# Optimization experiments

Hardware: AMD Instinct MI355X
Metric: run time of the kernel (lower is better)

The kernel has to match this reference:

```python
import jax, jax.numpy as jnp
import numpy as np

KERNEL = 25
PAD = (KERNEL - 1) // 2  # 12
LN_EPS = 1e-5
CAP_FACTOR = 2.0
K_VALUE = 2


def _moving_avg(x):
    # x: [B, L, D]; Autoformer moving_avg: replicate-pad ends, avg-pool k=25 stride 1
    front = jnp.repeat(x[:, :1, :], PAD, axis=1)
    end = jnp.repeat(x[:, -1:, :], PAD, axis=1)
    xp = jnp.concatenate([front, x, end], axis=1)            # [B, L+2*PAD, D]
    cs = jnp.cumsum(xp, axis=1)
    cs = jnp.concatenate([jnp.zeros_like(cs[:, :1]), cs], axis=1)
    return (cs[:, KERNEL:] - cs[:, :-KERNEL]) / KERNEL        # [B, L, D]


def _layernorm(h, g, b):
    mu = jnp.mean(h, axis=-1, keepdims=True)
    d = h - mu
    var = jnp.mean(d * d, axis=-1, keepdims=True)
    return d * jax.lax.rsqrt(var + LN_EPS) * g + b


def setup_inputs() -> dict:
    key = jax.random.key(0)
    ks = jax.random.split(key, 6)
    B, L, D, H, E = 32, 512, 512, 1024, 8
    sd_in = 1.0 / np.sqrt(D)
    sd_h = 1.0 / np.sqrt(H)
    return {
        "x": jax.random.normal(ks[0], (B, L, D), jnp.float32),
        "Wt": jax.random.normal(ks[1], (D, H), jnp.float32) * sd_in,
        "bt": jax.random.normal(ks[2], (H,), jnp.float32) * sd_in,
        "gt": jnp.ones((H,), jnp.float32),
        "bet": jnp.zeros((H,), jnp.float32),
        "Ws": jax.random.normal(ks[3], (D, H), jnp.float32) * sd_in,
        "bs": jax.random.normal(ks[4], (H,), jnp.float32) * sd_in,
        "gs": jnp.ones((H,), jnp.float32),
        "bes": jnp.zeros((H,), jnp.float32),
        "W2": jax.random.normal(ks[5], (H, E), jnp.float32) * sd_h,
        "b2": jnp.zeros((E,), jnp.float32),
    }


def reference(x, Wt, bt, gt, bet, Ws, bs, gs, bes, W2, b2):
    # series decomposition: (residual, moving_mean) -> (trend_init, seasonal_init)
    ma = _moving_avg(x)
    trend_init = x - ma          # residual (first return of series_decomp)
    seasonal_init = ma           # moving mean (second return)

    t = _layernorm(trend_init @ Wt + bt, gt, bet)       # [B, L, H]
    s = _layernorm(seasonal_init @ Ws + bs, gs, bes)    # [B, L, H]
    med = jax.nn.relu(t + s)
    logits = med @ W2 + b2                               # [B, L, E]
    gate_scores = jax.nn.softmax(logits, axis=-1)

    B, L, E = gate_scores.shape
    capacity = int(CAP_FACTOR * B)

    _, top_k_indices = jax.lax.top_k(gate_scores, K_VALUE)  # [B, L, K]
    # torch scatter_(1, idx, 1) on 3D: mask[b, idx[b,l,j], j] = 1
    bi = jnp.arange(B)[:, None, None]
    ji = jnp.arange(K_VALUE)[None, None, :]
    mask = jnp.zeros_like(gate_scores).at[bi, top_k_indices, ji].set(1.0)

    masked = gate_scores * mask
    denom = jnp.sum(masked, axis=0, keepdims=True) + 1e-4    # [1, L, E]
    return masked / denom * capacity
```

## Files before the change

kernel.cpp:

```cpp
#include <hip/hip_runtime.h>

#define NB 32
#define NL 512
#define ND 512
#define NH 1024
#define NE 8
#define NROWS (NB * NL)
#define CW 2048
#define SPAD 136

typedef __attribute__((ext_vector_type(8))) short bf16x8;
typedef __attribute__((ext_vector_type(4))) float f32x4;
typedef __attribute__((ext_vector_type(4))) unsigned u32x4;

__device__ __forceinline__ unsigned short f2bf(float f) {
    unsigned u = __float_as_uint(f);
    return (unsigned short)((u + 0x7fffu + ((u >> 16) & 1u)) >> 16);
}
__device__ __forceinline__ float bf2f(unsigned short b) {
    return __uint_as_float(((unsigned)b) << 16);
}
__device__ __forceinline__ unsigned pktr(float a, float b) {
    return (__float_as_uint(a) >> 16) | (__float_as_uint(b) & 0xFFFF0000u);
}

__global__ __launch_bounds__(256) void wprep(
    const float* __restrict__ Wt, const float* __restrict__ Ws,
    unsigned* __restrict__ bpack)
{
    __shared__ float tile[64][65];
    int bid = blockIdx.x;
    int mat = bid >> 7, rem = bid & 127;
    int kt0 = (rem >> 4) << 6;
    int nt0 = (rem & 15) << 6;
    const float* W = mat ? Ws : Wt;
    unsigned* Oh = bpack;
    unsigned* Ol = bpack + 524288u;
    int t = threadIdx.x;
    #pragma unroll
    for (int i = 0; i < 16; ++i) {
        int idx = t + 256 * i;
        int k = idx >> 6, n = idx & 63;
        tile[k][n] = W[(size_t)(kt0 + k) * NH + nt0 + n];
    }
    __syncthreads();
    #pragma unroll
    for (int i = 0; i < 8; ++i) {
        int idx = t + 256 * i;
        int jp = idx & 3, lane = (idx >> 2) & 63, kbr = (idx >> 8) & 1, ntr = (idx >> 9) & 3;
        int ncol = ntr * 16 + (lane & 15);
        int kcol = kbr * 32 + ((lane >> 4) << 3) + jp * 2;
        float w0 = tile[kcol][ncol], w1 = tile[kcol + 1][ncol];
        unsigned short h0 = f2bf(w0), h1 = f2bf(w1);
        unsigned short l0 = f2bf(w0 - bf2f(h0)), l1 = f2bf(w1 - bf2f(h1));
        int ntg = mat * 64 + (nt0 >> 4) + ntr;
        int kb = (kt0 >> 5) + kbr;
        unsigned offs = ((unsigned)(ntg * 16 + kb) * 64u + (unsigned)lane) * 4u + jp;
        Oh[offs] = (unsigned)h0 | ((unsigned)h1 << 16);
        Ol[offs] = (unsigned)l0 | ((unsigned)l1 << 16);
    }
}

__global__ __launch_bounds__(512, 4) void gemm_all(
    const float* __restrict__ x, const unsigned* __restrict__ bpack,
    unsigned short* __restrict__ C, unsigned short* __restrict__ Clo)
{
    __shared__ union {
        unsigned short A[2][128][64];
        unsigned short cs[64][264];
    } sm;

    const int tid = threadIdx.x, lane = tid & 63, wave = tid >> 6;
    const int g = lane >> 4, c = lane & 15;

    if (blockIdx.x < 1024) {
        const int wm = wave >> 2, wn = wave & 3;
        const int bid = blockIdx.x;
        const int xcd = bid & 7, idx = bid >> 3;
        const int mi = xcd * 16 + (idx >> 3), ni = idx & 7;
        const int m0 = mi * 128;

        const int srow = tid >> 2, sj = tid & 3;
        const int wcol = (sj * 8) ^ ((srow & 7) << 3);
        const float* xs = x + (size_t)(m0 + srow) * ND + sj * 8;

        f32x4 acc[4][4];
        #pragma unroll
        for (int nf = 0; nf < 4; ++nf)
            #pragma unroll
            for (int mf = 0; mf < 4; ++mf) acc[nf][mf] = (f32x4){0.f, 0.f, 0.f, 0.f};

        float4 xa = *(const float4*)xs;
        float4 xb = *(const float4*)(xs + 4);

        int p = 0;
        for (int kb = 0; kb < 16; ++kb) {
            u32x4 u;
            u.x = pktr(xa.x, xa.y); u.y = pktr(xa.z, xa.w);
            u.z = pktr(xb.x, xb.y); u.w = pktr(xb.z, xb.w);
            *(u32x4*)&sm.A[p][srow][wcol] = u;
            if (kb < 15) {
                const float* pn = xs + (kb + 1) * 32;
                xa = *(const float4*)pn;
                xb = *(const float4*)(pn + 4);
            }
            __syncthreads();

            bf16x8 af[4];
            #pragma unroll
            for (int mf = 0; mf < 4; ++mf) {
                int R = wm * 64 + mf * 16 + c;
                int rcol = (g * 8) ^ ((R & 7) << 3);
                af[mf] = *(const bf16x8*)&sm.A[p][R][rcol];
            }
            #pragma unroll
            for (int nf = 0; nf < 4; ++nf) {
                int nt = ni * 16 + wn * 4 + nf;
                bf16x8 bfr = *(const bf16x8*)(bpack + ((size_t)(nt * 16 + kb) * 64 + lane) * 4);
                #pragma unroll
                for (int mf = 0; mf < 4; ++mf)
                    acc[nf][mf] = __builtin_amdgcn_mfma_f32_16x16x32_bf16(af[mf], bfr, acc[nf][mf], 0, 0, 0);
            }
            p ^= 1;
        }

        #pragma unroll
        for (int ph = 0; ph < 2; ++ph) {
            __syncthreads();
            if (wm == ph) {
                #pragma unroll
                for (int nf = 0; nf < 4; ++nf)
                    #pragma unroll
                    for (int mf = 0; mf < 4; ++mf)
                        #pragma unroll
                        for (int r = 0; r < 4; ++r)
                            sm.cs[mf * 16 + g * 4 + r][wn * 64 + nf * 16 + c] =
                                (unsigned short)(__float_as_uint(acc[nf][mf][r]) >> 16);
            }
            __syncthreads();
            int row = tid >> 3, ch = tid & 7;
            int grow = m0 + ph * 64 + row;
            if ((grow & 511) >= 32) {
                unsigned short* dst = &C[(size_t)grow * CW + ni * 256 + ch * 32];
                #pragma unroll
                for (int q = 0; q < 4; ++q)
                    *(uint4*)(dst + q * 8) = *(const uint4*)&sm.cs[row][ch * 32 + q * 8];
            }
        }
    } else {
        const int eb = blockIdx.x - 1024;
        const int bq = eb >> 3, ni = eb & 7;
        const int m0 = bq * NL;
        const unsigned* Bhi = bpack;
        const unsigned* Blo = bpack + 524288u;

        f32x4 acc[4][2];
        #pragma unroll
        for (int nf = 0; nf < 4; ++nf)
            #pragma unroll
            for (int mf = 0; mf < 2; ++mf) acc[nf][mf] = (f32x4){0.f, 0.f, 0.f, 0.f};

        if (tid < 256) {
            const float* xr0 = x + (size_t)(m0 + c) * ND + g * 8;
            #pragma unroll 2
            for (int kb = 0; kb < 16; ++kb) {
                bf16x8 ah[2], al[2];
                #pragma unroll
                for (int mf = 0; mf < 2; ++mf) {
                    const float* p = xr0 + mf * (16 * ND) + kb * 32;
                    float4 a0 = *(const float4*)p;
                    float4 a1 = *(const float4*)(p + 4);
                    float f[8] = {a0.x, a0.y, a0.z, a0.w, a1.x, a1.y, a1.z, a1.w};
                    float lo[8];
                    #pragma unroll
                    for (int j = 0; j < 8; ++j) {
                        float hif = __uint_as_float(__float_as_uint(f[j]) & 0xFFFF0000u);
                        lo[j] = f[j] - hif;
                    }
                    u32x4 uh, ul;
                    uh.x = pktr(f[0], f[1]); uh.y = pktr(f[2], f[3]);
                    uh.z = pktr(f[4], f[5]); uh.w = pktr(f[6], f[7]);
                    ul.x = pktr(lo[0], lo[1]); ul.y = pktr(lo[2], lo[3]);
                    ul.z = pktr(lo[4], lo[5]); ul.w = pktr(lo[6], lo[7]);
                    ah[mf] = __builtin_bit_cast(bf16x8, uh);
                    al[mf] = __builtin_bit_cast(bf16x8, ul);
                }
                #pragma unroll
                for (int nf = 0; nf < 4; ++nf) {
                    int nt = ni * 16 + wave * 4 + nf;
                    size_t bo = ((size_t)(nt * 16 + kb) * 64 + lane) * 4;
                    bf16x8 bh = *(const bf16x8*)(Bhi + bo);
                    bf16x8 bl = *(const bf16x8*)(Blo + bo);
                    #pragma unroll
                    for (int mf = 0; mf < 2; ++mf) {
                        acc[nf][mf] = __builtin_amdgcn_mfma_f32_16x16x32_bf16(ah[mf], bh, acc[nf][mf], 0, 0, 0);
                        acc[nf][mf] = __builtin_amdgcn_mfma_f32_16x16x32_bf16(al[mf], bh, acc[nf][mf], 0, 0, 0);
                        acc[nf][mf] = __builtin_amdgcn_mfma_f32_16x16x32_bf16(ah[mf], bl, acc[nf][mf], 0, 0, 0);
                    }
                }
            }
            #pragma unroll
            for (int nf = 0; nf < 4; ++nf)
                #pragma unroll
                for (int mf = 0; mf < 2; ++mf)
                    #pragma unroll
                    for (int r = 0; r < 4; ++r)
                        sm.cs[mf * 16 + g * 4 + r][wave * 64 + nf * 16 + c] =
                            (unsigned short)(__float_as_uint(acc[nf][mf][r]) >> 16);
        }
        __syncthreads();
        if (tid < 256) {
            #pragma unroll
            for (int i = 0; i < 4; ++i) {
                int idx = tid + 256 * i;
                int row = idx >> 5, cg = idx & 31;
                *(uint4*)&C[(size_t)(m0 + row) * CW + ni * 256 + cg * 8] = *(const uint4*)&sm.cs[row][cg * 8];
            }
        }
        __syncthreads();
        if (tid < 256) {
            #pragma unroll
            for (int nf = 0; nf < 4; ++nf)
                #pragma unroll
                for (int mf = 0; mf < 2; ++mf)
                    #pragma unroll
                    for (int r = 0; r < 4; ++r) {
                        float v = acc[nf][mf][r];
                        float hif = __uint_as_float(__float_as_uint(v) & 0xFFFF0000u);
                        sm.cs[mf * 16 + g * 4 + r][wave * 64 + nf * 16 + c] =
                            (unsigned short)(__float_as_uint(v - hif) >> 16);
                    }
        }
        __syncthreads();
        if (tid < 256) {
            #pragma unroll
            for (int i = 0; i < 3; ++i) {
                int idx = tid + 256 * i;
                int row = idx >> 5, cg = idx & 31;
                if (row < 20)
                    *(uint4*)&Clo[((size_t)bq * 20 + row) * CW + ni * 256 + cg * 8] = *(const uint4*)&sm.cs[row][cg * 8];
            }
        }
    }
}

__global__ __launch_bounds__(256) void stats_all(
    const unsigned short* __restrict__ C, const unsigned short* __restrict__ Clo,
    const float* __restrict__ bt, const float* __restrict__ bs,
    float* __restrict__ rowpart, float* __restrict__ exstat)
{
    __shared__ unsigned short stg[88][SPAD];
    const int tid = threadIdx.x;

    if (blockIdx.x < 1024) {
        const int bid = blockIdx.x;
        const int q = bid & 3, lc = (bid >> 2) & 7, b = bid >> 5;
        const int l0 = lc * 64;
        const int cq = tid & 31, rg = tid >> 5;
        const float inv25 = 1.f / 25.f;

        float s[8], qa[8];
        #pragma unroll
        for (int r = 0; r < 8; ++r) { s[r] = 0.f; qa[r] = 0.f; }

        for (int ch = 0; ch < 4; ++ch) {
            int cb = q * 512 + ch * 128;
            __syncthreads();
            for (int i = tid; i < 1408; i += 256) {
                int si = i >> 4, cg = i & 15;
                int gl = l0 - 12 + si;
                gl = gl < 0 ? 0 : (gl > NL - 1 ? NL - 1 : gl);
                *(uint4*)&stg[si][cg * 8] = *(const uint4*)&C[(size_t)(b * NL + gl) * CW + cb + cg * 8];
            }
            __syncthreads();

            float bv[4];
            {
                float4 b4 = q < 2 ? *(const float4*)&bt[cb + cq * 4]
                                  : *(const float4*)&bs[cb - 1024 + cq * 4];
                bv[0] = b4.x; bv[1] = b4.y; bv[2] = b4.z; bv[3] = b4.w;
            }
            float run[4] = {0.f, 0.f, 0.f, 0.f};
            #pragma unroll
            for (int w = 0; w < 25; ++w) {
                ushort4 u = *(const ushort4*)&stg[rg * 8 + w][cq * 4];
                run[0] += bf2f(u.x); run[1] += bf2f(u.y); run[2] += bf2f(u.z); run[3] += bf2f(u.w);
            }
            #pragma unroll
            for (int rr = 0; rr < 8; ++rr) {
                if (rr > 0) {
                    ushort4 un = *(const ushort4*)&stg[rg * 8 + rr + 24][cq * 4];
                    ushort4 uo = *(const ushort4*)&stg[rg * 8 + rr - 1][cq * 4];
                    run[0] += bf2f(un.x) - bf2f(uo.x); run[1] += bf2f(un.y) - bf2f(uo.y);
                    run[2] += bf2f(un.z) - bf2f(uo.z); run[3] += bf2f(un.w) - bf2f(uo.w);
                }
                float pre[4];
                if (q < 2) {
                    ushort4 uc = *(const ushort4*)&stg[rg * 8 + rr + 12][cq * 4];
                    pre[0] = bf2f(uc.x) - run[0] * inv25 + bv[0];
                    pre[1] = bf2f(uc.y) - run[1] * inv25 + bv[1];
                    pre[2] = bf2f(uc.z) - run[2] * inv25 + bv[2];
                    pre[3] = bf2f(uc.w) - run[3] * inv25 + bv[3];
                } else {
                    pre[0] = run[0] * inv25 + bv[0];
                    pre[1] = run[1] * inv25 + bv[1];
                    pre[2] = run[2] * inv25 + bv[2];
                    pre[3] = run[3] * inv25 + bv[3];
                }
                s[rr]  += pre[0] + pre[1] + pre[2] + pre[3];
                qa[rr] += pre[0] * pre[0] + pre[1] * pre[1] + pre[2] * pre[2] + pre[3] * pre[3];
            }
        }

        #pragma unroll
        for (int rr = 0; rr < 8; ++rr)
            #pragma unroll
            for (int o = 1; o < 32; o <<= 1) {
                s[rr]  += __shfl_xor(s[rr], o);
                qa[rr] += __shfl_xor(qa[rr], o);
            }
        if (cq == 0) {
            #pragma unroll
            for (int rr = 0; rr < 8; ++rr) {
                size_t gr = (size_t)b * NL + l0 + rg * 8 + rr;
                rowpart[(gr * 4 + q) * 2 + 0] = s[rr];
                rowpart[(gr * 4 + q) * 2 + 1] = qa[rr];
            }
        }
    } else {
        const int inst = (blockIdx.x - 1024) * 4 + (tid >> 6);
        const int b = inst >> 3, chunk = inst & 7;
        const int t = tid & 63;
        const int c4 = chunk * 256 + t * 4;
        const bool isU = chunk < 4;
        const float inv25 = 1.f / 25.f;

        float bias[4];
        {
            float4 b4 = isU ? *(const float4*)&bt[c4] : *(const float4*)&bs[c4 - 1024];
            bias[0] = b4.x; bias[1] = b4.y; bias[2] = b4.z; bias[3] = b4.w;
        }
        float s[8], q[8];
        #pragma unroll
        for (int r = 0; r < 8; ++r) { s[r] = 0.f; q[r] = 0.f; }

        float cs[4] = {0, 0, 0, 0}, v0[4], keep[8][4];
        #pragma unroll
        for (int j = 0; j < 20; ++j) {
            ushort4 h  = *(const ushort4*)&C[(size_t)(b * NL + j) * CW + c4];
            ushort4 lo = *(const ushort4*)&Clo[((size_t)b * 20 + j) * CW + c4];
            float u[4] = {bf2f(h.x) + bf2f(lo.x), bf2f(h.y) + bf2f(lo.y),
                          bf2f(h.z) + bf2f(lo.z), bf2f(h.w) + bf2f(lo.w)};
            if (j == 0) {
                #pragma unroll
                for (int k = 0; k < 4; ++k) v0[k] = u[k];
            }
            if (j < 8) {
                #pragma unroll
                for (int k = 0; k < 4; ++k) keep[j][k] = u[k];
            }
            #pragma unroll
            for (int k = 0; k < 4; ++k) cs[k] += u[k];
            if (j >= 12) {
                const int l = j - 12;
                const float w0 = (float)(24 - j);
                #pragma unroll
                for (int k = 0; k < 4; ++k) {
                    float ma = (cs[k] + w0 * v0[k]) * inv25;
                    float pre = isU ? (keep[l][k] - ma + bias[k]) : (ma + bias[k]);
                    s[l] += pre;
                    q[l] += pre * pre;
                }
            }
        }
        #pragma unroll
        for (int r = 0; r < 8; ++r)
            #pragma unroll
            for (int o = 1; o < 64; o <<= 1) {
                s[r] += __shfl_xor(s[r], o);
                q[r] += __shfl_xor(q[r], o);
            }
        if (t == 0) {
            #pragma unroll
            for (int r = 0; r < 8; ++r) {
                exstat[(((size_t)b * 8 + chunk) * 8 + r) * 2 + 0] = s[r];
                exstat[(((size_t)b * 8 + chunk) * 8 + r) * 2 + 1] = q[r];
            }
        }
    }
}

__global__ __launch_bounds__(64) void exact_apply(
    const unsigned short* __restrict__ C, const unsigned short* __restrict__ Clo,
    const float* __restrict__ bt, const float* __restrict__ gt, const float* __restrict__ bet,
    const float* __restrict__ bs, const float* __restrict__ gs, const float* __restrict__ bes,
    const float* __restrict__ W2, const float* __restrict__ exstat,
    float* __restrict__ exlg)
{
    const int t = threadIdx.x;
    const int chunk = blockIdx.x & 7, b = blockIdx.x >> 3;
    const int h2 = chunk * 128 + t * 2;
    const float inv25 = 1.f / 25.f;

    float mu_t[8], rs_t[8], mu_s[8], rs_s[8];
    #pragma unroll
    for (int l = 0; l < 8; ++l) {
        float st = 0.f, qt = 0.f, ss = 0.f, qs = 0.f;
        #pragma unroll
        for (int ch = 0; ch < 4; ++ch) {
            st += exstat[(((size_t)b * 8 + ch) * 8 + l) * 2 + 0];
            qt += exstat[(((size_t)b * 8 + ch) * 8 + l) * 2 + 1];
            ss += exstat[(((size_t)b * 8 + 4 + ch) * 8 + l) * 2 + 0];
            qs += exstat[(((size_t)b * 8 + 4 + ch) * 8 + l) * 2 + 1];
        }
        mu_t[l] = st * (1.f / NH);
        rs_t[l] = rsqrtf(qt * (1.f / NH) - mu_t[l] * mu_t[l] + 1e-5f);
        mu_s[l] = ss * (1.f / NH);
        rs_s[l] = rsqrtf(qs * (1.f / NH) - mu_s[l] * mu_s[l] + 1e-5f);
    }

    float btv[2], gtv[2], bev[2], bsv[2], gsv[2], besv[2], w2r[2][NE];
    #pragma unroll
    for (int k = 0; k < 2; ++k) {
        int h = h2 + k;
        btv[k] = bt[h]; gtv[k] = gt[h]; bev[k] = bet[h];
        bsv[k] = bs[h]; gsv[k] = gs[h]; besv[k] = bes[h];
        const float4* wp = (const float4*)&W2[(size_t)h * NE];
        float4 a = wp[0], c2 = wp[1];
        w2r[k][0] = a.x;  w2r[k][1] = a.y;  w2r[k][2] = a.z;  w2r[k][3] = a.w;
        w2r[k][4] = c2.x; w2r[k][5] = c2.y; w2r[k][6] = c2.z; w2r[k][7] = c2.w;
    }

    float csU[2] = {0, 0}, csV[2] = {0, 0}, v0U[2], v0V[2], keepU[8][2];
    float lg[8][NE];
    #pragma unroll
    for (int l = 0; l < 8; ++l)
        #pragma unroll
        for (int e = 0; e < NE; ++e) lg[l][e] = 0.f;

    #pragma unroll
    for (int j = 0; j < 20; ++j) {
        size_t rb = (size_t)(b * NL + j) * CW;
        size_t lb = ((size_t)b * 20 + j) * CW;
        ushort2 hu  = *(const ushort2*)&C[rb + h2];
        ushort2 lu  = *(const ushort2*)&Clo[lb + h2];
        ushort2 hv  = *(const ushort2*)&C[rb + NH + h2];
        ushort2 lv  = *(const ushort2*)&Clo[lb + NH + h2];
        float u[2] = {bf2f(hu.x) + bf2f(lu.x), bf2f(hu.y) + bf2f(lu.y)};
        float v[2] = {bf2f(hv.x) + bf2f(lv.x), bf2f(hv.y) + bf2f(lv.y)};
        if (j == 0) {
            #pragma unroll
            for (int k = 0; k < 2; ++k) { v0U[k] = u[k]; v0V[k] = v[k]; }
        }
        if (j < 8) {
            #pragma unroll
            for (int k = 0; k < 2; ++k) keepU[j][k] = u[k];
        }
        #pragma unroll
        for (int k = 0; k < 2; ++k) { csU[k] += u[k]; csV[k] += v[k]; }
        if (j >= 12) {
            const int l = j - 12;
            const float w0 = (float)(24 - j);
            #pragma unroll
            for (int k = 0; k < 2; ++k) {
                float maU = (csU[k] + w0 * v0U[k]) * inv25;
                float maV = (csV[k] + w0 * v0V[k]) * inv25;
                float tn = ((keepU[l][k] - maU + btv[k]) - mu_t[l]) * rs_t[l] * gtv[k] + bev[k];
                float sn = ((maV + bsv[k]) - mu_s[l]) * rs_s[l] * gsv[k] + besv[k];
                float m = tn + sn; m = m > 0.f ? m : 0.f;
                #pragma unroll
                for (int e = 0; e < NE; ++e) lg[l][e] = fmaf(m, w2r[k][e], lg[l][e]);
            }
        }
    }
    #pragma unroll
    for (int l = 0; l < 8; ++l)
        #pragma unroll
        for (int e = 0; e < NE; ++e)
            #pragma unroll
            for (int o = 1; o < 64; o <<= 1)
                lg[l][e] += __shfl_xor(lg[l][e], o);
    if (t == 0) {
        #pragma unroll
        for (int l = 0; l < 8; ++l)
            #pragma unroll
            for (int e = 0; e < NE; ++e)
                exlg[(((size_t)b * 8 + chunk) * 8 + l) * NE + e] = lg[l][e];
    }
}

__global__ __launch_bounds__(256) void apply_k(
    const unsigned short* __restrict__ C,
    const float* __restrict__ bt, const float* __restrict__ gt, const float* __restrict__ bet,
    const float* __restrict__ bs, const float* __restrict__ gs, const float* __restrict__ bes,
    const float* __restrict__ W2, const float* __restrict__ rowpart,
    float* __restrict__ lgpart)
{
    __shared__ unsigned short stgU[88][SPAD];
    __shared__ unsigned short stgV[88][SPAD];
    __shared__ float4 rowstat[64];

    const int tid = threadIdx.x;
    const int bid = blockIdx.x;
    const int q = bid & 3, lc = (bid >> 2) & 7, b = bid >> 5;
    const int l0 = lc * 64;
    const int cq = tid & 31, rg = tid >> 5;
    const float inv25 = 1.f / 25.f;

    if (tid < 64) {
        size_t gr = (size_t)b * NL + l0 + tid;
        const float* p = &rowpart[gr * 8];
        float st = p[0] + p[2], qt = p[1] + p[3];
        float ss = p[4] + p[6], qs = p[5] + p[7];
        float mut = st * (1.f / NH), mus = ss * (1.f / NH);
        float vt = qt * (1.f / NH) - mut * mut;
        float vs = qs * (1.f / NH) - mus * mus;
        rowstat[tid] = make_float4(mut, rsqrtf(vt + 1e-5f), mus, rsqrtf(vs + 1e-5f));
    }

    float lgp[8][NE];
    #pragma unroll
    for (int r = 0; r < 8; ++r)
        #pragma unroll
        for (int e = 0; e < NE; ++e) lgp[r][e] = 0.f;

    for (int ch = 0; ch < 2; ++ch) {
        int hb = q * 256 + ch * 128;
        __syncthreads();
        for (int i = tid; i < 1408; i += 256) {
            int si = i >> 4, cg = i & 15;
            int gl = l0 - 12 + si;
            gl = gl < 0 ? 0 : (gl > NL - 1 ? NL - 1 : gl);
            size_t rb = (size_t)(b * NL + gl) * CW;
            *(uint4*)&stgU[si][cg * 8] = *(const uint4*)&C[rb + hb + cg * 8];
            *(uint4*)&stgV[si][cg * 8] = *(const uint4*)&C[rb + NH + hb + cg * 8];
        }
        __syncthreads();

        int col = hb + cq * 4;
        float4 btv = *(const float4*)&bt[col],  gtv = *(const float4*)&gt[col];
        float4 bev = *(const float4*)&bet[col], bsv = *(const float4*)&bs[col];
        float4 gsv = *(const float4*)&gs[col],  besv = *(const float4*)&bes[col];
        float btr[4] = {btv.x, btv.y, btv.z, btv.w};
        float gtr[4] = {gtv.x, gtv.y, gtv.z, gtv.w};
        float ber[4] = {bev.x, bev.y, bev.z, bev.w};
        float bsr[4] = {bsv.x, bsv.y, bsv.z, bsv.w};
        float gsr[4] = {gsv.x, gsv.y, gsv.z, gsv.w};
        float besr[4] = {besv.x, besv.y, besv.z, besv.w};
        float w2r[4][NE];
        #pragma unroll
        for (int j = 0; j < 4; ++j) {
            const float4* wp = (const float4*)&W2[(size_t)(col + j) * NE];
            float4 a = wp[0], c2 = wp[1];
            w2r[j][0] = a.x;  w2r[j][1] = a.y;  w2r[j][2] = a.z;  w2r[j][3] = a.w;
            w2r[j][4] = c2.x; w2r[j][5] = c2.y; w2r[j][6] = c2.z; w2r[j][7] = c2.w;
        }

        float runU[4] = {0.f, 0.f, 0.f, 0.f}, runV[4] = {0.f, 0.f, 0.f, 0.f};
        #pragma unroll
        for (int w = 0; w < 25; ++w) {
            ushort4 u = *(const ushort4*)&stgU[rg * 8 + w][cq * 4];
            ushort4 v = *(const ushort4*)&stgV[rg * 8 + w][cq * 4];
            runU[0] += bf2f(u.x); runU[1] += bf2f(u.y); runU[2] += bf2f(u.z); runU[3] += bf2f(u.w);
            runV[0] += bf2f(v.x); runV[1] += bf2f(v.y); runV[2] += bf2f(v.z); runV[3] += bf2f(v.w);
        }
        #pragma unroll
        for (int rr = 0; rr < 8; ++rr) {
            if (rr > 0) {
                ushort4 un = *(const ushort4*)&stgU[rg * 8 + rr + 24][cq * 4];
                ushort4 uo = *(const ushort4*)&stgU[rg * 8 + rr - 1][cq * 4];
                ushort4 vn = *(const ushort4*)&stgV[rg * 8 + rr + 24][cq * 4];
                ushort4 vo = *(const ushort4*)&stgV[rg * 8 + rr - 1][cq * 4];
                runU[0] += bf2f(un.x) - bf2f(uo.x); runU[1] += bf2f(un.y) - bf2f(uo.y);
                runU[2] += bf2f(un.z) - bf2f(uo.z); runU[3] += bf2f(un.w) - bf2f(uo.w);
                runV[0] += bf2f(vn.x) - bf2f(vo.x); runV[1] += bf2f(vn.y) - bf2f(vo.y);
                runV[2] += bf2f(vn.z) - bf2f(vo.z); runV[3] += bf2f(vn.w) - bf2f(vo.w);
            }
            float4 rs = rowstat[rg * 8 + rr];
            ushort4 uc = *(const ushort4*)&stgU[rg * 8 + rr + 12][cq * 4];
            float cen[4] = {bf2f(uc.x), bf2f(uc.y), bf2f(uc.z), bf2f(uc.w)};
            float med[4];
            #pragma unroll
            for (int j = 0; j < 4; ++j) {
                float tn = ((cen[j] - runU[j] * inv25 + btr[j]) - rs.x) * rs.y * gtr[j] + ber[j];
                float sn = ((runV[j] * inv25 + bsr[j]) - rs.z) * rs.w * gsr[j] + besr[j];
                float m = tn + sn;
                med[j] = m > 0.f ? m : 0.f;
            }
            #pragma unroll
            for (int e = 0; e < NE; ++e)
                lgp[rr][e] = fmaf(med[0], w2r[0][e], fmaf(med[1], w2r[1][e],
                             fmaf(med[2], w2r[2][e], fmaf(med[3], w2r[3][e], lgp[rr][e]))));
        }
    }

    #pragma unroll
    for (int rr = 0; rr < 8; ++rr)
        #pragma unroll
        for (int e = 0; e < NE; ++e)
            #pragma unroll
            for (int o = 1; o < 32; o <<= 1)
                lgp[rr][e] += __shfl_xor(lgp[rr][e], o);
    if (cq == 0) {
        #pragma unroll
        for (int rr = 0; rr < 8; ++rr) {
            size_t gr = (size_t)b * NL + l0 + rg * 8 + rr;
            #pragma unroll
            for (int e = 0; e < NE; ++e)
                lgpart[(gr * 4 + q) * NE + e] = lgp[rr][e];
        }
    }
}

__global__ __launch_bounds__(256) void final_all(
    const float* __restrict__ lgpart, const float* __restrict__ exlg,
    const float* __restrict__ b2,
    unsigned* __restrict__ mb, float* __restrict__ gates)
{
    const int t = threadIdx.x;
    if (blockIdx.x < 64) {
        int row = blockIdx.x * 256 + t;
        int b = row >> 9, l = row & (NL - 1);
        float lg[NE];
        #pragma unroll
        for (int e = 0; e < NE; ++e) lg[e] = b2[e];
        #pragma unroll
        for (int qq = 0; qq < 4; ++qq)
            #pragma unroll
            for (int e = 0; e < NE; ++e)
                lg[e] += lgpart[((size_t)row * 4 + qq) * NE + e];
        int i0 = 0;
        #pragma unroll
        for (int e = 1; e < NE; ++e) if (lg[e] > lg[i0]) i0 = e;
        int i1 = i0 == 0 ? 1 : 0;
        #pragma unroll
        for (int e = 0; e < NE; ++e) if (e != i0 && lg[e] > lg[i1]) i1 = e;
        unsigned m = (l < 8) ? 0u : ((1u << i0) | (1u << (8 + i1)));
        #pragma unroll
        for (int o = 1; o < 64; o <<= 1) m |= __shfl_xor(m, o);
        if ((t & 63) == 0) {
            atomicOr(&mb[2 * b + 0], m & 0xffu);
            atomicOr(&mb[2 * b + 1], m >> 8);
        }
    } else {
        const int b = t >> 3, l = t & 7;
        float lg[NE];
        #pragma unroll
        for (int e = 0; e < NE; ++e) lg[e] = b2[e];
        #pragma unroll
        for (int ch = 0; ch < 8; ++ch)
            #pragma unroll
            for (int e = 0; e < NE; ++e)
                lg[e] += exlg[(((size_t)b * 8 + ch) * 8 + l) * NE + e];
        float mx = lg[0];
        #pragma unroll
        for (int e = 1; e < NE; ++e) mx = lg[e] > mx ? lg[e] : mx;
        float p[NE]; float sum = 0.f;
        #pragma unroll
        for (int e = 0; e < NE; ++e) { p[e] = expf(lg[e] - mx); sum += p[e]; }
        float inv = 1.f / sum;
        #pragma unroll
        for (int e = 0; e < NE; ++e)
            gates[((size_t)b * 8 + l) * NE + e] = p[e] * inv;
        int i0 = 0;
        #pragma unroll
        for (int e = 1; e < NE; ++e) if (lg[e] > lg[i0]) i0 = e;
        int i1 = i0 == 0 ? 1 : 0;
        #pragma unroll
        for (int e = 0; e < NE; ++e) if (e != i0 && lg[e] > lg[i1]) i1 = e;
        unsigned m = (1u << i0) | (1u << (8 + i1));
        m |= __shfl_xor(m, 1); m |= __shfl_xor(m, 2); m |= __shfl_xor(m, 4);
        if (l == 0) {
            atomicOr(&mb[2 * b + 0], m & 0xffu);
            atomicOr(&mb[2 * b + 1], m >> 8);
        }
    }
}

__global__ void finalize_k(const unsigned* __restrict__ mb,
                           const float* __restrict__ gates,
                           float* __restrict__ out)
{
    int t = threadIdx.x;
    if (t >= 16) return;
    int l = t >> 1, e = t & 1;
    float m[NB];
    float sum = 0.f;
    #pragma unroll
    for (int bb = 0; bb < NB; ++bb) {
        float gvv = gates[((size_t)bb * 8 + l) * NE + e];
        float on  = ((mb[2 * bb + e] >> l) & 1u) ? 1.f : 0.f;
        m[bb] = gvv * on;
        sum += m[bb];
    }
    float scale = 64.f / (sum + 1e-4f);
    #pragma unroll
    for (int bb = 0; bb < NB; ++bb)
        out[(size_t)bb * (NL * NE) + l * NE + e] = m[bb] * scale;
}

extern "C" void kernel_launch(void* const* d_in, const int* in_sizes, int n_in,
                              void* d_out, int out_size, void* d_ws, size_t ws_size,
                              hipStream_t stream) {
    const float* x   = (const float*)d_in[0];
    const float* Wt  = (const float*)d_in[1];
    const float* bt  = (const float*)d_in[2];
    const float* gt  = (const float*)d_in[3];
    const float* bet = (const float*)d_in[4];
    const float* Ws  = (const float*)d_in[5];
    const float* bs  = (const float*)d_in[6];
    const float* gs  = (const float*)d_in[7];
    const float* bes = (const float*)d_in[8];
    const float* W2  = (const float*)d_in[9];
    const float* b2  = (const float*)d_in[10];
    float* out = (float*)d_out;

    char* wsb = (char*)d_ws;
    unsigned*       mbp     = (unsigned*)wsb;
    float*          gates   = (float*)(wsb + 256);
    unsigned*       bpack   = (unsigned*)(wsb + 4096);
    float*          rowpart = (float*)(wsb + 4096);
    float*          lgpart  = (float*)(wsb + 4096 + 524288);
    float*          exstat  = (float*)(wsb + 4096 + 524288 + 2097152);
    float*          exlg    = (float*)(wsb + 4096 + 524288 + 2097152 + 16384);
    unsigned short* C       = (unsigned short*)(wsb + 4096 + 4194304);
    unsigned short* Clo     = (unsigned short*)(wsb + 4096 + 4194304 + (size_t)NROWS * CW * 2);

    hipMemsetAsync(d_out, 0, sizeof(float) * NB * NL * NE, stream);
    hipMemsetAsync(mbp, 0, 256, stream);

    wprep<<<256, 256, 0, stream>>>(Wt, Ws, bpack);
    gemm_all<<<1280, 512, 0, stream>>>(x, bpack, C, Clo);
    stats_all<<<1088, 256, 0, stream>>>(C, Clo, bt, bs, rowpart, exstat);
    exact_apply<<<256, 64, 0, stream>>>(C, Clo, bt, gt, bet, bs, gs, bes, W2, exstat, exlg);
    apply_k<<<1024, 256, 0, stream>>>(C, bt, gt, bet, bs, gs, bes, W2, rowpart, lgpart);
    final_all<<<65, 256, 0, stream>>>(lgpart, exlg, b2, mbp, gates);
    finalize_k<<<1, 64, 0, stream>>>(mbp, gates, out);
}
```

Measured before the change: 176.5 us.

## Double GEMM block N-tile to 512 and use all waves in exact path

```diff
diff --git a/kernel.cpp b/kernel.cpp
--- a/kernel.cpp
+++ b/kernel.cpp
@@ -21,7 +21,7 @@
     return __uint_as_float(((unsigned)b) << 16);
 }
 __device__ __forceinline__ unsigned pktr(float a, float b) {
-    return (__float_as_uint(a) >> 16) | (__float_as_uint(b) & 0xFFFF0000u);
+    return __builtin_amdgcn_perm(__float_as_uint(b), __float_as_uint(a), 0x07060302u);
 }
 
 __global__ __launch_bounds__(256) void wprep(
@@ -73,22 +73,22 @@
     const int tid = threadIdx.x, lane = tid & 63, wave = tid >> 6;
     const int g = lane >> 4, c = lane & 15;
 
-    if (blockIdx.x < 1024) {
+    if (blockIdx.x < 512) {
         const int wm = wave >> 2, wn = wave & 3;
         const int bid = blockIdx.x;
         const int xcd = bid & 7, idx = bid >> 3;
-        const int mi = xcd * 16 + (idx >> 3), ni = idx & 7;
+        const int mi = xcd * 16 + (idx >> 2), ni = idx & 3;
         const int m0 = mi * 128;
+
+        f32x4 acc[8][4];
+        #pragma unroll
+        for (int nf = 0; nf < 8; ++nf)
+            #pragma unroll
+            for (int mf = 0; mf < 4; ++mf) acc[nf][mf] = (f32x4){0.f, 0.f, 0.f, 0.f};
 
         const int srow = tid >> 2, sj = tid & 3;
         const int wcol = (sj * 8) ^ ((srow & 7) << 3);
         const float* xs = x + (size_t)(m0 + srow) * ND + sj * 8;
-
-        f32x4 acc[4][4];
-        #pragma unroll
-        for (int nf = 0; nf < 4; ++nf)
-            #pragma unroll
-            for (int mf = 0; mf < 4; ++mf) acc[nf][mf] = (f32x4){0.f, 0.f, 0.f, 0.f};
 
         float4 xa = *(const float4*)xs;
         float4 xb = *(const float4*)(xs + 4);
@@ -114,8 +114,8 @@
                 af[mf] = *(const bf16x8*)&sm.A[p][R][rcol];
             }
             #pragma unroll
-            for (int nf = 0; nf < 4; ++nf) {
-                int nt = ni * 16 + wn * 4 + nf;
+            for (int nf = 0; nf < 8; ++nf) {
+                int nt = ni * 32 + wn * 8 + nf;
                 bf16x8 bfr = *(const bf16x8*)(bpack + ((size_t)(nt * 16 + kb) * 64 + lane) * 4);
                 #pragma unroll
                 for (int mf = 0; mf < 4; ++mf)
@@ -125,31 +125,33 @@
         }
 
         #pragma unroll
-        for (int ph = 0; ph < 2; ++ph) {
-            __syncthreads();
-            if (wm == ph) {
-                #pragma unroll
-                for (int nf = 0; nf < 4; ++nf)
+        for (int ph = 0; ph < 2; ++ph)
+            #pragma unroll
+            for (int chh = 0; chh < 2; ++chh) {
+                __syncthreads();
+                if (wm == ph && (wn >> 1) == chh) {
                     #pragma unroll
-                    for (int mf = 0; mf < 4; ++mf)
+                    for (int nf = 0; nf < 8; ++nf)
                         #pragma unroll
-                        for (int r = 0; r < 4; ++r)
-                            sm.cs[mf * 16 + g * 4 + r][wn * 64 + nf * 16 + c] =
-                                (unsigned short)(__float_as_uint(acc[nf][mf][r]) >> 16);
-            }
-            __syncthreads();
-            int row = tid >> 3, ch = tid & 7;
-            int grow = m0 + ph * 64 + row;
-            if ((grow & 511) >= 32) {
-                unsigned short* dst = &C[(size_t)grow * CW + ni * 256 + ch * 32];
-                #pragma unroll
-                for (int q = 0; q < 4; ++q)
-                    *(uint4*)(dst + q * 8) = *(const uint4*)&sm.cs[row][ch * 32 + q * 8];
-            }
-        }
+                        for (int mf = 0; mf < 4; ++mf)
+                            #pragma unroll
+                            for (int r = 0; r < 4; ++r)
+                                sm.cs[mf * 16 + g * 4 + r][(wn & 1) * 128 + nf * 16 + c] =
+                                    (unsigned short)(__float_as_uint(acc[nf][mf][r]) >> 16);
+                }
+                __syncthreads();
+                int row = tid >> 3, chv = tid & 7;
+                int grow = m0 + ph * 64 + row;
+                if ((grow & 511) >= 32) {
+                    unsigned short* dst = &C[(size_t)grow * CW + ni * 512 + chh * 256 + chv * 32];
+                    #pragma unroll
+                    for (int q = 0; q < 4; ++q)
+                        *(uint4*)(dst + q * 8) = *(const uint4*)&sm.cs[row][chv * 32 + q * 8];
+                }
+            }
     } else {
-        const int eb = blockIdx.x - 1024;
-        const int bq = eb >> 3, ni = eb & 7;
+        const int eb = blockIdx.x - 512;
+        const int bq = eb >> 2, nq = eb & 3;
         const int m0 = bq * NL;
         const unsigned* Bhi = bpack;
         const unsigned* Blo = bpack + 524288u;
@@ -160,85 +162,91 @@
             #pragma unroll
             for (int mf = 0; mf < 2; ++mf) acc[nf][mf] = (f32x4){0.f, 0.f, 0.f, 0.f};
 
-        if (tid < 256) {
-            const float* xr0 = x + (size_t)(m0 + c) * ND + g * 8;
-            #pragma unroll 2
-            for (int kb = 0; kb < 16; ++kb) {
-                bf16x8 ah[2], al[2];
+        const float* xr0 = x + (size_t)(m0 + c) * ND + g * 8;
+        #pragma unroll 2
+        for (int kb = 0; kb < 16; ++kb) {
+            bf16x8 ah[2], al[2];
+            #pragma unroll
+            for (int mf = 0; mf < 2; ++mf) {
+                const float* p = xr0 + mf * (16 * ND) + kb * 32;
+                float4 a0 = *(const float4*)p;
+                float4 a1 = *(const float4*)(p + 4);
+                float f[8] = {a0.x, a0.y, a0.z, a0.w, a1.x, a1.y, a1.z, a1.w};
+                float lo[8];
+                #pragma unroll
+                for (int j = 0; j < 8; ++j) {
+                    float hif = __uint_as_float(__float_as_uint(f[j]) & 0xFFFF0000u);
+                    lo[j] = f[j] - hif;
+                }
+                u32x4 uh, ul;
+                uh.x = pktr(f[0], f[1]); uh.y = pktr(f[2], f[3]);
+                uh.z = pktr(f[4], f[5]); uh.w = pktr(f[6], f[7]);
+                ul.x = pktr(lo[0], lo[1]); ul.y = pktr(lo[2], lo[3]);
+                ul.z = pktr(lo[4], lo[5]); ul.w = pktr(lo[6], lo[7]);
+                ah[mf] = __builtin_bit_cast(bf16x8, uh);
+                al[mf] = __builtin_bit_cast(bf16x8, ul);
+            }
+            #pragma unroll
+            for (int nf = 0; nf < 4; ++nf) {
+                int nt = nq * 32 + wave * 4 + nf;
+                size_t bo = ((size_t)(nt * 16 + kb) * 64 + lane) * 4;
+                bf16x8 bh = *(const bf16x8*)(Bhi + bo);
+                bf16x8 bl = *(const bf16x8*)(Blo + bo);
                 #pragma unroll
                 for (int mf = 0; mf < 2; ++mf) {
-                    const float* p = xr0 + mf * (16 * ND) + kb * 32;
-                    float4 a0 = *(const float4*)p;
-                    float4 a1 = *(const float4*)(p + 4);
-                    float f[8] = {a0.x, a0.y, a0.z, a0.w, a1.x, a1.y, a1.z, a1.w};
-                    float lo[8];
+                    acc[nf][mf] = __builtin_amdgcn_mfma_f32_16x16x32_bf16(ah[mf], bh, acc[nf][mf], 0, 0, 0);
+                    acc[nf][mf] = __builtin_amdgcn_mfma_f32_16x16x32_bf16(al[mf], bh, acc[nf][mf], 0, 0, 0);
+                    acc[nf][mf] = __builtin_amdgcn_mfma_f32_16x16x32_bf16(ah[mf], bl, acc[nf][mf], 0, 0, 0);
+                }
+            }
+        }
+
+        #pragma unroll
+        for (int ph = 0; ph < 2; ++ph) {
+            __syncthreads();
+            if ((wave >> 2) == ph) {
+                #pragma unroll
+                for (int nf = 0; nf < 4; ++nf)
                     #pragma unroll
-                    for (int j = 0; j < 8; ++j) {
-                        float hif = __uint_as_float(__float_as_uint(f[j]) & 0xFFFF0000u);
-                        lo[j] = f[j] - hif;
-                    }
-                    u32x4 uh, ul;
-                    uh.x = pktr(f[0], f[1]); uh.y = pktr(f[2], f[3]);
-                    uh.z = pktr(f[4], f[5]); uh.w = pktr(f[6], f[7]);
-                    ul.x = pktr(lo[0], lo[1]); ul.y = pktr(lo[2], lo[3]);
-                    ul.z = pktr(lo[4], lo[5]); ul.w = pktr(lo[6], lo[7]);
-                    ah[mf] = __builtin_bit_cast(bf16x8, uh);
-                    al[mf] = __builtin_bit_cast(bf16x8, ul);
-                }
-                #pragma unroll
-                for (int nf = 0; nf < 4; ++nf) {
-                    int nt = ni * 16 + wave * 4 + nf;
-                    size_t bo = ((size_t)(nt * 16 + kb) * 64 + lane) * 4;
-                    bf16x8 bh = *(const bf16x8*)(Bhi + bo);
-                    bf16x8 bl = *(const bf16x8*)(Blo + bo);
+                    for (int mf = 0; mf < 2; ++mf)
+                        #pragma unroll
+                        for (int r = 0; r < 4; ++r)
+                            sm.cs[mf * 16 + g * 4 + r][(wave & 3) * 64 + nf * 16 + c] =
+                                (unsigned short)(__float_as_uint(acc[nf][mf][r]) >> 16);
+            }
+            __syncthreads();
+            #pragma unroll
+            for (int i = 0; i < 2; ++i) {
+                int id = tid + 512 * i;
+                int row = id >> 5, cg = id & 31;
+                *(uint4*)&C[(size_t)(m0 + row) * CW + nq * 512 + ph * 256 + cg * 8] =
+                    *(const uint4*)&sm.cs[row][cg * 8];
+            }
+        }
+        #pragma unroll
+        for (int ph = 0; ph < 2; ++ph) {
+            __syncthreads();
+            if ((wave >> 2) == ph) {
+                #pragma unroll
+                for (int nf = 0; nf < 4; ++nf)
                     #pragma unroll
-                    for (int mf = 0; mf < 2; ++mf) {
-                        acc[nf][mf] = __builtin_amdgcn_mfma_f32_16x16x32_bf16(ah[mf], bh, acc[nf][mf], 0, 0, 0);
-                        acc[nf][mf] = __builtin_amdgcn_mfma_f32_16x16x32_bf16(al[mf], bh, acc[nf][mf], 0, 0, 0);
-                        acc[nf][mf] = __builtin_amdgcn_mfma_f32_16x16x32_bf16(ah[mf], bl, acc[nf][mf], 0, 0, 0);
-                    }
-                }
-            }
-            #pragma unroll
-            for (int nf = 0; nf < 4; ++nf)
-                #pragma unroll
-                for (int mf = 0; mf < 2; ++mf)
-                    #pragma unroll
-                    for (int r = 0; r < 4; ++r)
-                        sm.cs[mf * 16 + g * 4 + r][wave * 64 + nf * 16 + c] =
-                            (unsigned short)(__float_as_uint(acc[nf][mf][r]) >> 16);
-        }
-        __syncthreads();
-        if (tid < 256) {
-            #pragma unroll
-            for (int i = 0; i < 4; ++i) {
-                int idx = tid + 256 * i;
-                int row = idx >> 5, cg = idx & 31;
-                *(uint4*)&C[(size_t)(m0 + row) * CW + ni * 256 + cg * 8] = *(const uint4*)&sm.cs[row][cg * 8];
-            }
-        }
-        __syncthreads();
-        if (tid < 256) {
-            #pragma unroll
-            for (int nf = 0; nf < 4; ++nf)
-                #pragma unroll
-                for (int mf = 0; mf < 2; ++mf)
-                    #pragma unroll
-                    for (int r = 0; r < 4; ++r) {
-                        float v = acc[nf][mf][r];
-                        float hif = __uint_as_float(__float_as_uint(v) & 0xFFFF0000u);
-                        sm.cs[mf * 16 + g * 4 + r][wave * 64 + nf * 16 + c] =
-                            (unsigned short)(__float_as_uint(v - hif) >> 16);
-                    }
-        }
-        __syncthreads();
-        if (tid < 256) {
-            #pragma unroll
-            for (int i = 0; i < 3; ++i) {
-                int idx = tid + 256 * i;
-                int row = idx >> 5, cg = idx & 31;
+                    for (int mf = 0; mf < 2; ++mf)
+                        #pragma unroll
+                        for (int r = 0; r < 4; ++r) {
+                            float v = acc[nf][mf][r];
+                            float hif = __uint_as_float(__float_as_uint(v) & 0xFFFF0000u);
+                            sm.cs[mf * 16 + g * 4 + r][(wave & 3) * 64 + nf * 16 + c] =
+                                (unsigned short)(__float_as_uint(v - hif) >> 16);
+                        }
+            }
+            __syncthreads();
+            #pragma unroll
+            for (int i = 0; i < 2; ++i) {
+                int id = tid + 512 * i;
+                int row = id >> 5, cg = id & 31;
                 if (row < 20)
-                    *(uint4*)&Clo[((size_t)bq * 20 + row) * CW + ni * 256 + cg * 8] = *(const uint4*)&sm.cs[row][cg * 8];
+                    *(uint4*)&Clo[((size_t)bq * 20 + row) * CW + nq * 512 + ph * 256 + cg * 8] =
+                        *(const uint4*)&sm.cs[row][cg * 8];
             }
         }
     }
@@ -730,7 +738,7 @@
     hipMemsetAsync(mbp, 0, 256, stream);
 
     wprep<<<256, 256, 0, stream>>>(Wt, Ws, bpack);
-    gemm_all<<<1280, 512, 0, stream>>>(x, bpack, C, Clo);
+    gemm_all<<<640, 512, 0, stream>>>(x, bpack, C, Clo);
     stats_all<<<1088, 256, 0, stream>>>(C, Clo, bt, bs, rowpart, exstat);
     exact_apply<<<256, 64, 0, stream>>>(C, Clo, bt, gt, bet, bs, gs, bes, W2, exstat, exlg);
     apply_k<<<1024, 256, 0, stream>>>(C, bt, gt, bet, bs, gs, bes, W2, rowpart, lgpart);
```

After: 366.2 us. +107.6%, slower.
